# Kernel tuning notes

Measured on AMD Instinct MI355X. Metric: run time of the kernel, lower is better.

Reference implementation:

```python
import jax, jax.numpy as jnp
import numpy as np
import math

N = 100000      # nodes
E = 1600000     # edges (before self-loops)
F_IN = 512      # input features
H = 64          # hidden
C = 40          # classes
L = 4           # GCNII layers
ALPHA = 0.1
LAMDA = 0.5


def setup_inputs() -> dict:
    key = jax.random.key(0)
    ks = jax.random.split(key, 8)
    x = jax.random.normal(ks[0], (N, F_IN), jnp.float32)
    edge_index = jax.random.randint(ks[1], (2, E), 0, N)
    edge_weight = jax.random.uniform(ks[2], (E,), jnp.float32)
    W_in = jax.random.normal(ks[3], (F_IN, H), jnp.float32) * 0.05
    b_in = jnp.zeros((H,), jnp.float32)
    W_layers = jax.random.normal(ks[4], (L, H, H), jnp.float32) * 0.1
    W_out = jax.random.normal(ks[5], (H, C), jnp.float32) * 0.1
    b_out = jnp.zeros((C,), jnp.float32)
    return dict(x=x, edge_index=edge_index, edge_weight=edge_weight,
                W_in=W_in, b_in=b_in, W_layers=W_layers, W_out=W_out, b_out=b_out)


def _gcn_norm(edge_index, edge_weight, n):
    """Add self-loops (weight 1) and compute symmetric normalization D^-1/2 A D^-1/2."""
    loop = jnp.arange(n)
    src = jnp.concatenate([edge_index[0], loop])
    dst = jnp.concatenate([edge_index[1], loop])
    w = jnp.concatenate([edge_weight, jnp.ones((n,), edge_weight.dtype)])
    deg = jax.ops.segment_sum(w, dst, num_segments=n)
    dinv = jnp.where(deg > 0, jax.lax.rsqrt(deg), jnp.zeros_like(deg))
    norm = dinv[src] * w * dinv[dst]  # [E+N]
    return src, dst, norm


def reference(x, edge_index, edge_weight, W_in, b_in, W_layers, W_out, b_out):
    n = x.shape[0]
    src, dst, norm = _gcn_norm(edge_index, edge_weight, n)
    # input projection (dropout is identity in eval mode)
    h = jax.nn.relu(x @ W_in + b_in)  # [N, H]
    h0 = h
    for i in range(W_layers.shape[0]):
        beta = math.log(LAMDA / (i + 1) + 1.0)
        # sparse propagate: Ahat @ h via gather + segment_sum
        agg = jax.ops.segment_sum(norm[:, None] * h[src], dst, num_segments=n)  # [N, H]
        support = (1.0 - ALPHA) * agg + ALPHA * h0  # initial residual
        # identity mapping: beta * support @ W + (1 - beta) * support
        h = jax.nn.relu(beta * (support @ W_layers[i]) + (1.0 - beta) * support)
    out = h @ W_out + b_out  # [N, C]
    return jax.nn.log_softmax(out, axis=1)
```

## Files before the change

### kernel.cpp

```cpp
#include <hip/hip_runtime.h>
#include <math.h>

#define HD 64
#define FIN 512
#define NC 40

struct __align__(8) EdgeT { int s; float v; };

typedef __attribute__((ext_vector_type(8))) short bf16x8;
typedef __attribute__((ext_vector_type(8))) unsigned short u16x8;
typedef __attribute__((ext_vector_type(4))) float f32x4;

__device__ __forceinline__ float bf2f(ushort u) {
    return __uint_as_float(((unsigned int)u) << 16);
}
__device__ __forceinline__ ushort f2bf(float f) {
    unsigned int u = __float_as_uint(f);
    unsigned int r = (u + 0x7fffu + ((u >> 16) & 1u)) >> 16;
    return (ushort)r;
}


__global__ __launch_bounds__(256) void prep_kernel(unsigned long long* packed8, int n,
        const float* __restrict__ Win, ushort* __restrict__ Wf,
        const float* __restrict__ Wlay, ushort* __restrict__ Wf2, int L,
        const float* __restrict__ Wo, const float* __restrict__ bo,
        float* __restrict__ Wo_pad, float* __restrict__ bo_pad) {
    int i = blockIdx.x * 256 + threadIdx.x;
    if (i < 8 * n) packed8[i] = (i < n) ? (1ULL << 32) : 0ULL;
    if (i < FIN * HD) {
        int j = i & 7, l = (i >> 3) & 63, t = (i >> 9) & 3, c = i >> 11;
        int k = c * 32 + ((l >> 4) * 8) + j;
        Wf[i] = f2bf(Win[k * HD + t * 16 + (l & 15)]);
    }
    if (i < L * HD * HD) {
        int li = i >> 12, ii = i & 4095;
        int j = ii & 7, l = (ii >> 3) & 63, t = (ii >> 9) & 3, c = (ii >> 11) & 1;
        int k = c * 32 + ((l >> 4) * 8) + j;
        Wf2[i] = f2bf(Wlay[(size_t)li * HD * HD + k * HD + t * 16 + (l & 15)]);
    }
    if (i < HD * HD) {
        int k = i >> 6, c2 = i & 63;
        Wo_pad[i] = (c2 < NC) ? Wo[k * NC + c2] : 0.f;
    }
    if (i < HD) bo_pad[i] = (i < NC) ? bo[i] : 0.f;
}


__global__ __launch_bounds__(256) void histproj_kernel(
        const int* __restrict__ dst, const float* __restrict__ w,
        unsigned long long* packed8, ushort* __restrict__ rank, int E, int n,
        const float* __restrict__ x, const ushort* __restrict__ Wf,
        const float* __restrict__ bias, ushort* __restrict__ h0, int npb) {
    if ((int)blockIdx.x >= npb) {
        int i = (blockIdx.x - npb) * 256 + threadIdx.x;
        if (i < E) {
            int d = dst[i];
            int c = i & 7;
            unsigned long long add = (1ULL << 48) |
                (unsigned long long)(w[i] * 4294967296.0f);
            unsigned long long old = atomicAdd(&packed8[(size_t)c * n + d], add);
            rank[i] = (ushort)(old >> 48);
        }
        return;
    }
    const int lane = threadIdx.x & 63;
    const int wave = threadIdx.x >> 6;
    const int row = lane & 15;
    const int g = lane >> 4;
    const int base = blockIdx.x * 64 + wave * 16;

    f32x4 acc[4];
#pragma unroll
    for (int t = 0; t < 4; ++t) acc[t] = (f32x4){0.f, 0.f, 0.f, 0.f};

    int nodeA = base + row;
    if (nodeA >= n) nodeA = n - 1;
    const float* xr = x + (size_t)nodeA * FIN + g * 8;

    for (int c = 0; c < 16; ++c) {
        bf16x8 afr;
        float4 v0 = *(const float4*)(xr + c * 32);
        float4 v1 = *(const float4*)(xr + c * 32 + 4);
        afr[0] = (short)f2bf(v0.x); afr[1] = (short)f2bf(v0.y);
        afr[2] = (short)f2bf(v0.z); afr[3] = (short)f2bf(v0.w);
        afr[4] = (short)f2bf(v1.x); afr[5] = (short)f2bf(v1.y);
        afr[6] = (short)f2bf(v1.z); afr[7] = (short)f2bf(v1.w);
#pragma unroll
        for (int t = 0; t < 4; ++t) {
            bf16x8 bfr = *(const bf16x8*)(Wf + ((size_t)(c * 4 + t) * 64 + lane) * 8);
            acc[t] = __builtin_amdgcn_mfma_f32_16x16x32_bf16(afr, bfr, acc[t], 0, 0, 0);
        }
    }

    float bj[4];
#pragma unroll
    for (int t = 0; t < 4; ++t) bj[t] = bias[t * 16 + row];
#pragma unroll
    for (int r = 0; r < 4; ++r) {
        int node = base + g * 4 + r;
        if (node < n) {
#pragma unroll
            for (int t = 0; t < 4; ++t) {
                float v = fmaxf(acc[t][r] + bj[t], 0.f);
                h0[(size_t)node * HD + t * 16 + row] = f2bf(v);
            }
        }
    }
}

__global__ __launch_bounds__(256) void post_kernel(const unsigned long long* __restrict__ packed8,
        float* __restrict__ dinv, uint2* __restrict__ cbase,
        int* __restrict__ row_ptr, int* __restrict__ bsums, int n) {
    __shared__ int s[256];
    const unsigned long long M = 0xFFFFFFFFFFFFULL;
    int t = threadIdx.x;
    int i = blockIdx.x * 256 + t;
    int cnt = 0;
    if (i < n) {
        int c[8];
        unsigned long long fx = 0;
#pragma unroll
        for (int k = 0; k < 8; ++k) {
            unsigned long long p = packed8[(size_t)k * n + i];
            c[k] = (int)(p >> 48);
            fx += (p & M);
        }
        float deg = (float)((double)fx * (1.0 / 4294967296.0));
        dinv[i] = rsqrtf(deg);
        int b = 0; uint lo = 0, hi = 0;
#pragma unroll
        for (int k = 0; k < 4; ++k) { lo |= ((uint)b) << (8 * k); b += c[k]; }
#pragma unroll
        for (int k = 0; k < 4; ++k) { hi |= ((uint)b) << (8 * k); b += c[4 + k]; }
        cbase[i] = make_uint2(lo, hi);
        cnt = b;
    }
    s[t] = cnt; __syncthreads();
    for (int off = 1; off < 256; off <<= 1) {
        int u = (t >= off) ? s[t - off] : 0;
        __syncthreads();
        s[t] += u;
        __syncthreads();
    }
    if (i < n) row_ptr[i] = s[t] - cnt;
    if (t == 255) bsums[blockIdx.x] = s[255];
}

__global__ __launch_bounds__(512) void scan_top_kernel(int* bsums, int nb) {
    __shared__ int s[512];
    int t = threadIdx.x;
    int v = (t < nb) ? bsums[t] : 0;
    s[t] = v; __syncthreads();
    for (int off = 1; off < 512; off <<= 1) {
        int u = (t >= off) ? s[t - off] : 0;
        __syncthreads();
        s[t] += u;
        __syncthreads();
    }
    if (t < nb) bsums[t] = s[t] - v;
}

__global__ __launch_bounds__(256) void scan_add_kernel(int* __restrict__ row_ptr,
        const int* __restrict__ bsums, int n, int E) {
    int i = blockIdx.x * 256 + threadIdx.x;
    if (i < n) row_ptr[i] += bsums[blockIdx.x];
    if (i == 0) row_ptr[n] = E;
}

__global__ __launch_bounds__(256) void scatter_kernel(const int* __restrict__ src,
        const int* __restrict__ dst, const float* __restrict__ w,
        const float* __restrict__ dinv, const int* __restrict__ row_ptr,
        const uint2* __restrict__ cbase, const ushort* __restrict__ rank,
        EdgeT* __restrict__ ed, int E) {
    int i = blockIdx.x * 256 + threadIdx.x;
    if (i < E) {
        int s = src[i], d = dst[i];
        int c = i & 7;
        uint2 cb = cbase[d];
        int base = (int)(((c < 4) ? (cb.x >> (8 * c)) : (cb.y >> (8 * (c - 4)))) & 0xffu);
        int pos = row_ptr[d] + base + (int)rank[i];
        EdgeT e; e.s = s; e.v = dinv[s] * w[i] * dinv[d];
        ed[pos] = e;
    }
}


__global__ __launch_bounds__(256) void spmm_kernel(const ushort* __restrict__ h_in,
        ushort* __restrict__ agg, const float* __restrict__ dinv,
        const int* __restrict__ row_ptr, const EdgeT* __restrict__ ed, int n) {
    const int lane = threadIdx.x & 63;
    const int g = lane >> 3;
    const int fl = (lane & 7) * 8;
    int oct = (blockIdx.x * 256 + threadIdx.x) >> 6;
    int node = oct * 8 + g;
    bool valid = node < n;
    int nc = valid ? node : n - 1;

    float di = dinv[nc];
    float sw = di * di;
    u16x8 us = *(const u16x8*)(h_in + (size_t)nc * HD + fl);
    float a[8], b[8];
#pragma unroll
    for (int j = 0; j < 8; ++j) { a[j] = sw * bf2f((ushort)us[j]); b[j] = 0.f; }

    int e = row_ptr[nc], end = row_ptr[nc + 1];
    for (; e + 4 <= end; e += 4) {
        EdgeT E0 = ed[e], E1 = ed[e + 1], E2 = ed[e + 2], E3 = ed[e + 3];
        u16x8 u0 = *(const u16x8*)(h_in + (size_t)E0.s * HD + fl);
        u16x8 u1 = *(const u16x8*)(h_in + (size_t)E1.s * HD + fl);
        u16x8 u2 = *(const u16x8*)(h_in + (size_t)E2.s * HD + fl);
        u16x8 u3 = *(const u16x8*)(h_in + (size_t)E3.s * HD + fl);
#pragma unroll
        for (int j = 0; j < 8; ++j) {
            a[j] = fmaf(E0.v, bf2f((ushort)u0[j]), a[j]);
            b[j] = fmaf(E1.v, bf2f((ushort)u1[j]), b[j]);
            a[j] = fmaf(E2.v, bf2f((ushort)u2[j]), a[j]);
            b[j] = fmaf(E3.v, bf2f((ushort)u3[j]), b[j]);
        }
    }
    for (; e < end; ++e) {
        EdgeT E0 = ed[e];
        u16x8 u0 = *(const u16x8*)(h_in + (size_t)E0.s * HD + fl);
#pragma unroll
        for (int j = 0; j < 8; ++j) a[j] = fmaf(E0.v, bf2f((ushort)u0[j]), a[j]);
    }

    if (valid) {
        u16x8 r;
#pragma unroll
        for (int j = 0; j < 8; ++j) r[j] = f2bf(a[j] + b[j]);
        *(u16x8*)(agg + (size_t)node * HD + fl) = r;
    }
}


__global__ __launch_bounds__(256) void lgemmm_kernel(const ushort* __restrict__ agg,
        const ushort* __restrict__ h0, const ushort* __restrict__ Wf2,
        ushort* __restrict__ C, int n, float beta) {
    const int lane = threadIdx.x & 63;
    const int wave = threadIdx.x >> 6;
    const int row = lane & 15;
    const int g = lane >> 4;
    const int base = blockIdx.x * 128 + wave * 32;
    const float ombeta = 1.f - beta;

    f32x4 acc[2][4];
#pragma unroll
    for (int m = 0; m < 2; ++m)
#pragma unroll
        for (int t = 0; t < 4; ++t) acc[m][t] = (f32x4){0.f, 0.f, 0.f, 0.f};

    bf16x8 afr[2][2];
#pragma unroll
    for (int m = 0; m < 2; ++m) {
        int node = base + m * 16 + row;
        if (node >= n) node = n - 1;
#pragma unroll
        for (int c = 0; c < 2; ++c) {
            u16x8 ua = *(const u16x8*)(agg + (size_t)node * HD + c * 32 + g * 8);
            u16x8 uh = *(const u16x8*)(h0 + (size_t)node * HD + c * 32 + g * 8);
#pragma unroll
            for (int j = 0; j < 8; ++j)
                afr[m][c][j] = (short)f2bf(fmaf(0.9f, bf2f((ushort)ua[j]),
                                                0.1f * bf2f((ushort)uh[j])));
        }
    }
#pragma unroll
    for (int c = 0; c < 2; ++c) {
#pragma unroll
        for (int t = 0; t < 4; ++t) {
            bf16x8 bfr = *(const bf16x8*)(Wf2 + ((size_t)(c * 4 + t) * 64 + lane) * 8);
            acc[0][t] = __builtin_amdgcn_mfma_f32_16x16x32_bf16(afr[0][c], bfr, acc[0][t], 0, 0, 0);
            acc[1][t] = __builtin_amdgcn_mfma_f32_16x16x32_bf16(afr[1][c], bfr, acc[1][t], 0, 0, 0);
        }
    }

#pragma unroll
    for (int m = 0; m < 2; ++m)
#pragma unroll
        for (int r = 0; r < 4; ++r) {
            int node = base + m * 16 + g * 4 + r;
            if (node < n) {
                ushort rr[4];
#pragma unroll
                for (int t = 0; t < 4; ++t) {
                    int idx = (int)((size_t)0) + t * 16 + row;
                    float sa = bf2f(agg[(size_t)node * HD + idx]);
                    float sh = bf2f(h0[(size_t)node * HD + idx]);
                    float sup = fmaf(0.9f, sa, 0.1f * sh);
                    rr[t] = f2bf(fmaxf(fmaf(beta, acc[m][t][r], ombeta * sup), 0.f));
                }
#pragma unroll
                for (int t = 0; t < 4; ++t)
                    C[(size_t)node * HD + t * 16 + row] = rr[t];
            }
        }
}


__global__ __launch_bounds__(256) void outg_kernel(const ushort* __restrict__ A,
        const float* __restrict__ W, const float* __restrict__ bias,
        float* __restrict__ outp, int n) {
    __shared__ float Af[64 * 68];
    __shared__ float Wl[64 * 64];
    const int tid = threadIdx.x;
    const int tx = tid & 15;
    const int ty = tid >> 4;
    const int base = blockIdx.x * 64;
    const int kq = (tid & 15) * 4;
    const int rw = tid >> 4;

#pragma unroll
    for (int p = 0; p < 4; ++p) {
        int row = rw + p * 16;
        int ng = base + row; if (ng >= n) ng = n - 1;
        ushort4 u = *(const ushort4*)(A + (size_t)ng * HD + kq);
        Af[row * 68 + kq + 0] = bf2f(u.x);
        Af[row * 68 + kq + 1] = bf2f(u.y);
        Af[row * 68 + kq + 2] = bf2f(u.z);
        Af[row * 68 + kq + 3] = bf2f(u.w);
        *(float4*)(Wl + row * 64 + kq) =
            *(const float4*)(W + (size_t)row * HD + kq);
    }
    __syncthreads();

    float acc[4][4];
#pragma unroll
    for (int i = 0; i < 4; ++i)
#pragma unroll
        for (int j = 0; j < 4; ++j) acc[i][j] = 0.f;

#pragma unroll
    for (int kk = 0; kk < 64; kk += 4) {
        float4 a4[4];
#pragma unroll
        for (int i = 0; i < 4; ++i)
            a4[i] = *(const float4*)(Af + (ty * 4 + i) * 68 + kk);
#pragma unroll
        for (int k2 = 0; k2 < 4; ++k2) {
            float w[4];
            *(float4*)w = *(const float4*)(Wl + (kk + k2) * 64 + tx * 4);
#pragma unroll
            for (int i = 0; i < 4; ++i) {
                float a = ((const float*)&a4[i])[k2];
#pragma unroll
                for (int j = 0; j < 4; ++j) acc[i][j] = fmaf(a, w[j], acc[i][j]);
            }
        }
    }

    float b[4];
#pragma unroll
    for (int j = 0; j < 4; ++j) b[j] = bias[tx * 4 + j];
    const bool valid = (tx < 10);
#pragma unroll
    for (int i = 0; i < 4; ++i) {
        float lo[4];
        float m = -3.0e38f;
#pragma unroll
        for (int j = 0; j < 4; ++j) {
            lo[j] = acc[i][j] + b[j];
            if (valid) m = fmaxf(m, lo[j]);
        }
#pragma unroll
        for (int off = 1; off < 16; off <<= 1)
            m = fmaxf(m, __shfl_xor(m, off, 64));
        float s = 0.f;
        if (valid) {
#pragma unroll
            for (int j = 0; j < 4; ++j) s += __expf(lo[j] - m);
        }
#pragma unroll
        for (int off = 1; off < 16; off <<= 1)
            s += __shfl_xor(s, off, 64);
        float lse = __logf(s);
        int ng = base + ty * 4 + i;
        if (ng < n && valid) {
            float4 r;
            r.x = lo[0] - m - lse; r.y = lo[1] - m - lse;
            r.z = lo[2] - m - lse; r.w = lo[3] - m - lse;
            *(float4*)(outp + (size_t)ng * NC + tx * 4) = r;
        }
    }
}


extern "C" void kernel_launch(void* const* d_in, const int* in_sizes, int n_in,
                              void* d_out, int out_size, void* d_ws, size_t ws_size,
                              hipStream_t stream) {
    const float* x        = (const float*)d_in[0];
    const int*   eidx     = (const int*)d_in[1];
    const float* ew       = (const float*)d_in[2];
    const float* W_in     = (const float*)d_in[3];
    const float* b_in     = (const float*)d_in[4];
    const float* W_layers = (const float*)d_in[5];
    const float* W_out    = (const float*)d_in[6];
    const float* b_out    = (const float*)d_in[7];
    float* out = (float*)d_out;

    const int N = in_sizes[0] / FIN;
    const int E = in_sizes[2];
    const int L = in_sizes[5] / (HD * HD);
    const int* src = eidx;
    const int* dst = eidx + E;

    size_t off = 0;
    auto carve = [&](size_t bytes) {
        void* p = (char*)d_ws + off;
        off += (bytes + 255) & ~(size_t)255;
        return p;
    };
    unsigned long long* packed8 = (unsigned long long*)carve((size_t)N * 8 * 8);
    float*  dinv    = (float*)carve((size_t)N * 4);
    uint2*  cbase   = (uint2*)carve((size_t)N * 8);
    int*    row_ptr = (int*)  carve((size_t)(N + 1) * 4);
    int*    bsums   = (int*)  carve(512 * 4);
    float*  Wo_pad  = (float*)carve((size_t)HD * HD * 4);
    float*  bo_pad  = (float*)carve((size_t)HD * 4);
    ushort* Wf      = (ushort*)carve((size_t)FIN * HD * 2);
    ushort* Wf2     = (ushort*)carve((size_t)L * HD * HD * 2);
    ushort* rank    = (ushort*)carve((size_t)E * 2);
    EdgeT*  ed      = (EdgeT*)carve((size_t)E * 8);
    ushort* h0      = (ushort*)carve((size_t)N * HD * 2);
    ushort* hA      = (ushort*)carve((size_t)N * HD * 2);
    ushort* hB      = (ushort*)carve((size_t)N * HD * 2);
    (void)ws_size;

    const int NB = (N + 255) / 256;
    const int EB = (E + 255) / 256;
    const int NPB = (N + 63) / 64;

    prep_kernel<<<(8 * N + 255) / 256, 256, 0, stream>>>(packed8, N, W_in, Wf,
                                                         W_layers, Wf2, L,
                                                         W_out, b_out, Wo_pad, bo_pad);
    histproj_kernel<<<NPB + EB, 256, 0, stream>>>(dst, ew, packed8, rank, E, N,
                                                  x, Wf, b_in, h0, NPB);
    post_kernel<<<NB, 256, 0, stream>>>(packed8, dinv, cbase, row_ptr, bsums, N);
    scan_top_kernel<<<1, 512, 0, stream>>>(bsums, NB);
    scan_add_kernel<<<NB, 256, 0, stream>>>(row_ptr, bsums, N, E);
    scatter_kernel<<<EB, 256, 0, stream>>>(src, dst, ew, dinv, row_ptr, cbase, rank, ed, E);

    const int nocts = (N + 7) / 8;
    const int SB = (nocts + 3) / 4;
    const int LB = (N + 127) / 128;
    const ushort* cur = h0;
    ushort* bufs[2] = { hA, hB };
    for (int i = 0; i < L; ++i) {
        float beta = logf(0.5f / (float)(i + 1) + 1.0f);
        ushort* sup = bufs[i & 1];
        spmm_kernel<<<SB, 256, 0, stream>>>(cur, sup, dinv, row_ptr, ed, N);
        lgemmm_kernel<<<LB, 256, 0, stream>>>(sup, h0, Wf2 + (size_t)i * HD * HD,
                                              sup, N, beta);
        cur = sup;
    }

    outg_kernel<<<(N + 63) / 64, 256, 0, stream>>>(cur, Wo_pad, bo_pad, out, N);
}
```

Baseline: 401.5 us.

## Fuse SpMM with layer GEMM via LDS and use MFMA for output head

Merges the sparse aggregation and the per-layer dense MFMA GEMM into one kernel. Each wave aggregates 32 nodes, folds in the initial residual, stores the support tile in shared memory, and runs the MFMA transform from there. This removes the intermediate agg write/read and one launch per layer. The output projection moves from an FP32 LDS GEMM to bf16 MFMA with a fused log-softmax. The trade-off is lower parallelism per wave in the gather phase (4 sequential node groups per wave) and bf16 precision for the output weights.

```diff
diff --git a/kernel.cpp b/kernel.cpp
--- a/kernel.cpp
+++ b/kernel.cpp
@@ -25,7 +25,7 @@
         const float* __restrict__ Win, ushort* __restrict__ Wf,
         const float* __restrict__ Wlay, ushort* __restrict__ Wf2, int L,
         const float* __restrict__ Wo, const float* __restrict__ bo,
-        float* __restrict__ Wo_pad, float* __restrict__ bo_pad) {
+        ushort* __restrict__ Wfo, float* __restrict__ bo_pad) {
     int i = blockIdx.x * 256 + threadIdx.x;
     if (i < 8 * n) packed8[i] = (i < n) ? (1ULL << 32) : 0ULL;
     if (i < FIN * HD) {
@@ -40,8 +40,10 @@
         Wf2[i] = f2bf(Wlay[(size_t)li * HD * HD + k * HD + t * 16 + (l & 15)]);
     }
     if (i < HD * HD) {
-        int k = i >> 6, c2 = i & 63;
-        Wo_pad[i] = (c2 < NC) ? Wo[k * NC + c2] : 0.f;
+        int j = i & 7, l = (i >> 3) & 63, t = (i >> 9) & 3, c = (i >> 11) & 1;
+        int k = c * 32 + ((l >> 4) * 8) + j;
+        int col = t * 16 + (l & 15);
+        Wfo[i] = (col < NC) ? f2bf(Wo[k * NC + col]) : (ushort)0;
     }
     if (i < HD) bo_pad[i] = (i < NC) ? bo[i] : 0.f;
 }
@@ -186,64 +188,112 @@
 }
 
 
-__global__ __launch_bounds__(256) void spmm_kernel(const ushort* __restrict__ h_in,
-        ushort* __restrict__ agg, const float* __restrict__ dinv,
-        const int* __restrict__ row_ptr, const EdgeT* __restrict__ ed, int n) {
+__global__ __launch_bounds__(256) void layerm_kernel(const ushort* __restrict__ h_in,
+        const ushort* __restrict__ h0, ushort* __restrict__ h_out,
+        const ushort* __restrict__ Wf2, const float* __restrict__ dinv,
+        const int* __restrict__ row_ptr, const EdgeT* __restrict__ ed,
+        float beta, int n) {
+    __shared__ ushort S[4][32 * 72];
     const int lane = threadIdx.x & 63;
-    const int g = lane >> 3;
+    const int wave = threadIdx.x >> 6;
+    ushort* Sw = S[wave];
+    const int wbase = (blockIdx.x * 4 + wave) * 32;
+    const int gs = lane >> 3;
     const int fl = (lane & 7) * 8;
-    int oct = (blockIdx.x * 256 + threadIdx.x) >> 6;
-    int node = oct * 8 + g;
-    bool valid = node < n;
-    int nc = valid ? node : n - 1;
-
-    float di = dinv[nc];
-    float sw = di * di;
-    u16x8 us = *(const u16x8*)(h_in + (size_t)nc * HD + fl);
-    float a[8], b[8];
-#pragma unroll
-    for (int j = 0; j < 8; ++j) { a[j] = sw * bf2f((ushort)us[j]); b[j] = 0.f; }
-
-    int e = row_ptr[nc], end = row_ptr[nc + 1];
-    for (; e + 4 <= end; e += 4) {
-        EdgeT E0 = ed[e], E1 = ed[e + 1], E2 = ed[e + 2], E3 = ed[e + 3];
-        u16x8 u0 = *(const u16x8*)(h_in + (size_t)E0.s * HD + fl);
-        u16x8 u1 = *(const u16x8*)(h_in + (size_t)E1.s * HD + fl);
-        u16x8 u2 = *(const u16x8*)(h_in + (size_t)E2.s * HD + fl);
-        u16x8 u3 = *(const u16x8*)(h_in + (size_t)E3.s * HD + fl);
-#pragma unroll
-        for (int j = 0; j < 8; ++j) {
-            a[j] = fmaf(E0.v, bf2f((ushort)u0[j]), a[j]);
-            b[j] = fmaf(E1.v, bf2f((ushort)u1[j]), b[j]);
-            a[j] = fmaf(E2.v, bf2f((ushort)u2[j]), a[j]);
-            b[j] = fmaf(E3.v, bf2f((ushort)u3[j]), b[j]);
-        }
-    }
-    for (; e < end; ++e) {
-        EdgeT E0 = ed[e];
-        u16x8 u0 = *(const u16x8*)(h_in + (size_t)E0.s * HD + fl);
-#pragma unroll
-        for (int j = 0; j < 8; ++j) a[j] = fmaf(E0.v, bf2f((ushort)u0[j]), a[j]);
-    }
-
-    if (valid) {
+
+#pragma unroll
+    for (int p = 0; p < 4; ++p) {
+        int node = wbase + p * 8 + gs;
+        int nc = (node < n) ? node : n - 1;
+        float di = dinv[nc];
+        float sw = di * di;
+        u16x8 us = *(const u16x8*)(h_in + (size_t)nc * HD + fl);
+        float a[8], b[8];
+#pragma unroll
+        for (int j = 0; j < 8; ++j) { a[j] = sw * bf2f((ushort)us[j]); b[j] = 0.f; }
+
+        int e = row_ptr[nc], end = row_ptr[nc + 1];
+        for (; e + 4 <= end; e += 4) {
+            EdgeT E0 = ed[e], E1 = ed[e + 1], E2 = ed[e + 2], E3 = ed[e + 3];
+            u16x8 u0 = *(const u16x8*)(h_in + (size_t)E0.s * HD + fl);
+            u16x8 u1 = *(const u16x8*)(h_in + (size_t)E1.s * HD + fl);
+            u16x8 u2 = *(const u16x8*)(h_in + (size_t)E2.s * HD + fl);
+            u16x8 u3 = *(const u16x8*)(h_in + (size_t)E3.s * HD + fl);
+#pragma unroll
+            for (int j = 0; j < 8; ++j) {
+                a[j] = fmaf(E0.v, bf2f((ushort)u0[j]), a[j]);
+                b[j] = fmaf(E1.v, bf2f((ushort)u1[j]), b[j]);
+                a[j] = fmaf(E2.v, bf2f((ushort)u2[j]), a[j]);
+                b[j] = fmaf(E3.v, bf2f((ushort)u3[j]), b[j]);
+            }
+        }
+        for (; e < end; ++e) {
+            EdgeT E0 = ed[e];
+            u16x8 u0 = *(const u16x8*)(h_in + (size_t)E0.s * HD + fl);
+#pragma unroll
+            for (int j = 0; j < 8; ++j) a[j] = fmaf(E0.v, bf2f((ushort)u0[j]), a[j]);
+        }
+
+        u16x8 uh = *(const u16x8*)(h0 + (size_t)nc * HD + fl);
         u16x8 r;
 #pragma unroll
-        for (int j = 0; j < 8; ++j) r[j] = f2bf(a[j] + b[j]);
-        *(u16x8*)(agg + (size_t)node * HD + fl) = r;
-    }
-}
-
-
-__global__ __launch_bounds__(256) void lgemmm_kernel(const ushort* __restrict__ agg,
-        const ushort* __restrict__ h0, const ushort* __restrict__ Wf2,
-        ushort* __restrict__ C, int n, float beta) {
+        for (int j = 0; j < 8; ++j)
+            r[j] = f2bf(fmaf(0.9f, a[j] + b[j], 0.1f * bf2f((ushort)uh[j])));
+        *(u16x8*)(Sw + (p * 8 + gs) * 72 + fl) = r;
+    }
+
+    asm volatile("s_waitcnt lgkmcnt(0)" ::: "memory");
+    __builtin_amdgcn_wave_barrier();
+    __builtin_amdgcn_sched_barrier(0);
+
+    const int row = lane & 15;
+    const int g = lane >> 4;
+    f32x4 acc[2][4];
+#pragma unroll
+    for (int m = 0; m < 2; ++m)
+#pragma unroll
+        for (int t = 0; t < 4; ++t) acc[m][t] = (f32x4){0.f, 0.f, 0.f, 0.f};
+
+#pragma unroll
+    for (int c = 0; c < 2; ++c) {
+        bf16x8 afr[2];
+#pragma unroll
+        for (int m = 0; m < 2; ++m)
+            afr[m] = *(const bf16x8*)(Sw + (m * 16 + row) * 72 + c * 32 + g * 8);
+#pragma unroll
+        for (int t = 0; t < 4; ++t) {
+            bf16x8 bfr = *(const bf16x8*)(Wf2 + ((size_t)(c * 4 + t) * 64 + lane) * 8);
+            acc[0][t] = __builtin_amdgcn_mfma_f32_16x16x32_bf16(afr[0], bfr, acc[0][t], 0, 0, 0);
+            acc[1][t] = __builtin_amdgcn_mfma_f32_16x16x32_bf16(afr[1], bfr, acc[1][t], 0, 0, 0);
+        }
+    }
+
+    const float ombeta = 1.f - beta;
+#pragma unroll
+    for (int m = 0; m < 2; ++m)
+#pragma unroll
+        for (int r = 0; r < 4; ++r) {
+            int node = wbase + m * 16 + g * 4 + r;
+            if (node < n) {
+#pragma unroll
+                for (int t = 0; t < 4; ++t) {
+                    float sup = bf2f(Sw[(m * 16 + g * 4 + r) * 72 + t * 16 + row]);
+                    float v = fmaxf(fmaf(beta, acc[m][t][r], ombeta * sup), 0.f);
+                    h_out[(size_t)node * HD + t * 16 + row] = f2bf(v);
+                }
+            }
+        }
+}
+
+
+__global__ __launch_bounds__(256) void outm_kernel(const ushort* __restrict__ A,
+        const ushort* __restrict__ Wfo, const float* __restrict__ bo_pad,
+        float* __restrict__ outp, int n) {
     const int lane = threadIdx.x & 63;
     const int wave = threadIdx.x >> 6;
     const int row = lane & 15;
     const int g = lane >> 4;
     const int base = blockIdx.x * 128 + wave * 32;
-    const float ombeta = 1.f - beta;
 
     f32x4 acc[2][4];
 #pragma unroll
@@ -251,138 +301,53 @@
 #pragma unroll
         for (int t = 0; t < 4; ++t) acc[m][t] = (f32x4){0.f, 0.f, 0.f, 0.f};
 
-    bf16x8 afr[2][2];
-#pragma unroll
-    for (int m = 0; m < 2; ++m) {
-        int node = base + m * 16 + row;
-        if (node >= n) node = n - 1;
-#pragma unroll
-        for (int c = 0; c < 2; ++c) {
-            u16x8 ua = *(const u16x8*)(agg + (size_t)node * HD + c * 32 + g * 8);
-            u16x8 uh = *(const u16x8*)(h0 + (size_t)node * HD + c * 32 + g * 8);
-#pragma unroll
-            for (int j = 0; j < 8; ++j)
-                afr[m][c][j] = (short)f2bf(fmaf(0.9f, bf2f((ushort)ua[j]),
-                                                0.1f * bf2f((ushort)uh[j])));
-        }
-    }
 #pragma unroll
     for (int c = 0; c < 2; ++c) {
+        bf16x8 afr[2];
+#pragma unroll
+        for (int m = 0; m < 2; ++m) {
+            int node = base + m * 16 + row;
+            if (node >= n) node = n - 1;
+            afr[m] = *(const bf16x8*)(A + (size_t)node * HD + c * 32 + g * 8);
+        }
 #pragma unroll
         for (int t = 0; t < 4; ++t) {
-            bf16x8 bfr = *(const bf16x8*)(Wf2 + ((size_t)(c * 4 + t) * 64 + lane) * 8);
-            acc[0][t] = __builtin_amdgcn_mfma_f32_16x16x32_bf16(afr[0][c], bfr, acc[0][t], 0, 0, 0);
-            acc[1][t] = __builtin_amdgcn_mfma_f32_16x16x32_bf16(afr[1][c], bfr, acc[1][t], 0, 0, 0);
-        }
-    }
-
+            bf16x8 bfr = *(const bf16x8*)(Wfo + ((size_t)(c * 4 + t) * 64 + lane) * 8);
+            acc[0][t] = __builtin_amdgcn_mfma_f32_16x16x32_bf16(afr[0], bfr, acc[0][t], 0, 0, 0);
+            acc[1][t] = __builtin_amdgcn_mfma_f32_16x16x32_bf16(afr[1], bfr, acc[1][t], 0, 0, 0);
+        }
+    }
+
+    float bj[4];
+#pragma unroll
+    for (int t = 0; t < 4; ++t) bj[t] = bo_pad[t * 16 + row];
+    const bool v2 = (row < 8);
 #pragma unroll
     for (int m = 0; m < 2; ++m)
 #pragma unroll
         for (int r = 0; r < 4; ++r) {
+            float lo[3];
+            lo[0] = acc[m][0][r] + bj[0];
+            lo[1] = acc[m][1][r] + bj[1];
+            lo[2] = acc[m][2][r] + bj[2];
+            float mx = fmaxf(lo[0], lo[1]);
+            if (v2) mx = fmaxf(mx, lo[2]);
+#pragma unroll
+            for (int off = 1; off < 16; off <<= 1)
+                mx = fmaxf(mx, __shfl_xor(mx, off, 64));
+            float s = __expf(lo[0] - mx) + __expf(lo[1] - mx);
+            if (v2) s += __expf(lo[2] - mx);
+#pragma unroll
+            for (int off = 1; off < 16; off <<= 1)
+                s += __shfl_xor(s, off, 64);
+            float lse = __logf(s);
             int node = base + m * 16 + g * 4 + r;
             if (node < n) {
-                ushort rr[4];
-#pragma unroll
-                for (int t = 0; t < 4; ++t) {
-                    int idx = (int)((size_t)0) + t * 16 + row;
-                    float sa = bf2f(agg[(size_t)node * HD + idx]);
-                    float sh = bf2f(h0[(size_t)node * HD + idx]);
-                    float sup = fmaf(0.9f, sa, 0.1f * sh);
-                    rr[t] = f2bf(fmaxf(fmaf(beta, acc[m][t][r], ombeta * sup), 0.f));
-                }
-#pragma unroll
-                for (int t = 0; t < 4; ++t)
-                    C[(size_t)node * HD + t * 16 + row] = rr[t];
+                outp[(size_t)node * NC + row] = lo[0] - mx - lse;
+                outp[(size_t)node * NC + 16 + row] = lo[1] - mx - lse;
+                if (v2) outp[(size_t)node * NC + 32 + row] = lo[2] - mx - lse;
             }
         }
-}
-
-
-__global__ __launch_bounds__(256) void outg_kernel(const ushort* __restrict__ A,
-        const float* __restrict__ W, const float* __restrict__ bias,
-        float* __restrict__ outp, int n) {
-    __shared__ float Af[64 * 68];
-    __shared__ float Wl[64 * 64];
-    const int tid = threadIdx.x;
-    const int tx = tid & 15;
-    const int ty = tid >> 4;
-    const int base = blockIdx.x * 64;
-    const int kq = (tid & 15) * 4;
-    const int rw = tid >> 4;
-
-#pragma unroll
-    for (int p = 0; p < 4; ++p) {
-        int row = rw + p * 16;
-        int ng = base + row; if (ng >= n) ng = n - 1;
-        ushort4 u = *(const ushort4*)(A + (size_t)ng * HD + kq);
-        Af[row * 68 + kq + 0] = bf2f(u.x);
-        Af[row * 68 + kq + 1] = bf2f(u.y);
-        Af[row * 68 + kq + 2] = bf2f(u.z);
-        Af[row * 68 + kq + 3] = bf2f(u.w);
-        *(float4*)(Wl + row * 64 + kq) =
-            *(const float4*)(W + (size_t)row * HD + kq);
-    }
-    __syncthreads();
-
-    float acc[4][4];
-#pragma unroll
-    for (int i = 0; i < 4; ++i)
-#pragma unroll
-        for (int j = 0; j < 4; ++j) acc[i][j] = 0.f;
-
-#pragma unroll
-    for (int kk = 0; kk < 64; kk += 4) {
-        float4 a4[4];
-#pragma unroll
-        for (int i = 0; i < 4; ++i)
-            a4[i] = *(const float4*)(Af + (ty * 4 + i) * 68 + kk);
-#pragma unroll
-        for (int k2 = 0; k2 < 4; ++k2) {
-            float w[4];
-            *(float4*)w = *(const float4*)(Wl + (kk + k2) * 64 + tx * 4);
-#pragma unroll
-            for (int i = 0; i < 4; ++i) {
-                float a = ((const float*)&a4[i])[k2];
-#pragma unroll
-                for (int j = 0; j < 4; ++j) acc[i][j] = fmaf(a, w[j], acc[i][j]);
-            }
-        }
-    }
-
-    float b[4];
-#pragma unroll
-    for (int j = 0; j < 4; ++j) b[j] = bias[tx * 4 + j];
-    const bool valid = (tx < 10);
-#pragma unroll
-    for (int i = 0; i < 4; ++i) {
-        float lo[4];
-        float m = -3.0e38f;
-#pragma unroll
-        for (int j = 0; j < 4; ++j) {
-            lo[j] = acc[i][j] + b[j];
-            if (valid) m = fmaxf(m, lo[j]);
-        }
-#pragma unroll
-        for (int off = 1; off < 16; off <<= 1)
-            m = fmaxf(m, __shfl_xor(m, off, 64));
-        float s = 0.f;
-        if (valid) {
-#pragma unroll
-            for (int j = 0; j < 4; ++j) s += __expf(lo[j] - m);
-        }
-#pragma unroll
-        for (int off = 1; off < 16; off <<= 1)
-            s += __shfl_xor(s, off, 64);
-        float lse = __logf(s);
-        int ng = base + ty * 4 + i;
-        if (ng < n && valid) {
-            float4 r;
-            r.x = lo[0] - m - lse; r.y = lo[1] - m - lse;
-            r.z = lo[2] - m - lse; r.w = lo[3] - m - lse;
-            *(float4*)(outp + (size_t)ng * NC + tx * 4) = r;
-        }
-    }
 }
 
 
@@ -416,10 +381,10 @@
     uint2*  cbase   = (uint2*)carve((size_t)N * 8);
     int*    row_ptr = (int*)  carve((size_t)(N + 1) * 4);
     int*    bsums   = (int*)  carve(512 * 4);
-    float*  Wo_pad  = (float*)carve((size_t)HD * HD * 4);
     float*  bo_pad  = (float*)carve((size_t)HD * 4);
     ushort* Wf      = (ushort*)carve((size_t)FIN * HD * 2);
     ushort* Wf2     = (ushort*)carve((size_t)L * HD * HD * 2);
+    ushort* Wfo     = (ushort*)carve((size_t)HD * HD * 2);
     ushort* rank    = (ushort*)carve((size_t)E * 2);
     EdgeT*  ed      = (EdgeT*)carve((size_t)E * 8);
     ushort* h0      = (ushort*)carve((size_t)N * HD * 2);
@@ -433,7 +398,7 @@
 
     prep_kernel<<<(8 * N + 255) / 256, 256, 0, stream>>>(packed8, N, W_in, Wf,
                                                          W_layers, Wf2, L,
-                                                         W_out, b_out, Wo_pad, bo_pad);
+                                                         W_out, b_out, Wfo, bo_pad);
     histproj_kernel<<<NPB + EB, 256, 0, stream>>>(dst, ew, packed8, rank, E, N,
                                                   x, Wf, b_in, h0, NPB);
     post_kernel<<<NB, 256, 0, stream>>>(packed8, dinv, cbase, row_ptr, bsums, N);
@@ -441,19 +406,16 @@
     scan_add_kernel<<<NB, 256, 0, stream>>>(row_ptr, bsums, N, E);
     scatter_kernel<<<EB, 256, 0, stream>>>(src, dst, ew, dinv, row_ptr, cbase, rank, ed, E);
 
-    const int nocts = (N + 7) / 8;
-    const int SB = (nocts + 3) / 4;
     const int LB = (N + 127) / 128;
     const ushort* cur = h0;
     ushort* bufs[2] = { hA, hB };
     for (int i = 0; i < L; ++i) {
         float beta = logf(0.5f / (float)(i + 1) + 1.0f);
-        ushort* sup = bufs[i & 1];
-        spmm_kernel<<<SB, 256, 0, stream>>>(cur, sup, dinv, row_ptr, ed, N);
-        lgemmm_kernel<<<LB, 256, 0, stream>>>(sup, h0, Wf2 + (size_t)i * HD * HD,
-                                              sup, N, beta);
-        cur = sup;
-    }
-
-    outg_kernel<<<(N + 63) / 64, 256, 0, stream>>>(cur, Wo_pad, bo_pad, out, N);
-}
+        ushort* nxt = bufs[i & 1];
+        layerm_kernel<<<LB, 256, 0, stream>>>(cur, h0, nxt, Wf2 + (size_t)i * HD * HD,
+                                              dinv, row_ptr, ed, beta, N);
+        cur = nxt;
+    }
+
+    outm_kernel<<<LB, 256, 0, stream>>>(cur, Wfo, bo_pad, out, N);
+}
```

Result: faster. 348.3 us (-13.3%).
